# Kernel tuning notes

Hardware: AMD Instinct MI355X
Metric: run time of the kernel (lower is better)

## Reference

```python
import jax, jax.numpy as jnp
import numpy as np

N, E, F, D, G = 50000, 800000, 64, 64, 512
BN_EPS = 1e-5


def setup_inputs() -> dict:
    key = jax.random.key(0)
    ks = jax.random.split(key, 12)
    inp = {
        "x": jax.random.normal(ks[0], (N, F), dtype=jnp.float32),
        "edge_index": jax.random.randint(ks[1], (2, E), 0, N, dtype=jnp.int32),
        "batch": jnp.sort(jax.random.randint(ks[2], (N,), 0, G, dtype=jnp.int32)),
    }
    s = 0.05
    inp.update({
        "w1_a": jax.random.normal(ks[3], (F, D), jnp.float32) * s, "b1_a": jnp.zeros((D,), jnp.float32),
        "w1_b": jax.random.normal(ks[4], (D, D), jnp.float32) * s, "b1_b": jnp.zeros((D,), jnp.float32),
        "g1": jnp.ones((D,), jnp.float32), "be1": jnp.zeros((D,), jnp.float32),
        "w2_a": jax.random.normal(ks[5], (D, D), jnp.float32) * s, "b2_a": jnp.zeros((D,), jnp.float32),
        "w2_b": jax.random.normal(ks[6], (D, D), jnp.float32) * s, "b2_b": jnp.zeros((D,), jnp.float32),
        "g2": jnp.ones((D,), jnp.float32), "be2": jnp.zeros((D,), jnp.float32),
        "w3_a": jax.random.normal(ks[7], (D, D), jnp.float32) * s, "b3_a": jnp.zeros((D,), jnp.float32),
        "w3_b": jax.random.normal(ks[8], (D, D), jnp.float32) * s, "b3_b": jnp.zeros((D,), jnp.float32),
        "g3": jnp.ones((D,), jnp.float32), "be3": jnp.zeros((D,), jnp.float32),
        "w_lin0": jax.random.normal(ks[9], (D, 2 * D), jnp.float32) * s, "b_lin0": jnp.zeros((2 * D,), jnp.float32),
        "w_fc1": jax.random.normal(ks[10], (2 * D, D), jnp.float32) * s, "b_fc1": jnp.zeros((D,), jnp.float32),
    })
    return inp


def _gin_bn_layer(h, edge_index, w_a, b_a, w_b, b_b, gamma, beta):
    # GINConv (eps=0): nn(x + sum_{j->i} x_j); message = x[src] scattered to dst
    agg = jax.ops.segment_sum(h[edge_index[0]], edge_index[1], num_segments=h.shape[0])
    z = agg + h
    z = jnp.maximum(z @ w_a + b_a, 0.0) @ w_b + b_b  # inner MLP
    z = jnp.maximum(z, 0.0)                           # F.relu after conv
    mean = jnp.mean(z, axis=0)                        # BatchNorm1d, training stats
    var = jnp.mean((z - mean) ** 2, axis=0)
    return (z - mean) * jax.lax.rsqrt(var + BN_EPS) * gamma + beta


def reference(x, edge_index, batch,
              w1_a, b1_a, w1_b, b1_b, g1, be1,
              w2_a, b2_a, w2_b, b2_b, g2, be2,
              w3_a, b3_a, w3_b, b3_b, g3, be3,
              w_lin0, b_lin0, w_fc1, b_fc1):
    h = _gin_bn_layer(x, edge_index, w1_a, b1_a, w1_b, b1_b, g1, be1)
    h = _gin_bn_layer(h, edge_index, w2_a, b2_a, w2_b, b2_b, g2, be2)
    h = _gin_bn_layer(h, edge_index, w3_a, b3_a, w3_b, b3_b, g3, be3)
    xpool = jax.ops.segment_sum(h, batch, num_segments=G)  # global_add_pool [G, D]
    out = xpool @ w_lin0 + b_lin0                           # GINEncoder.lin0 -> [G, 2D]
    out = jnp.maximum(out @ w_fc1 + b_fc1, 0.0)             # relu(fc1); fc2 output is discarded (show_embedding=True)
    return out
```

## Files before the change

### kernel.cpp

```cpp
#include <hip/hip_runtime.h>

#define NN 50000
#define EE 800000
#define DD 64
#define GG 512
#define TILES 782
#define SCAN_BLOCKS 98

typedef __attribute__((ext_vector_type(8))) short short8;
typedef __attribute__((ext_vector_type(4))) float f32x4;

__device__ __forceinline__ float b2f(unsigned short u) {
    union { unsigned int i; float f; } c;
    c.i = ((unsigned int)u) << 16;
    return c.f;
}
__device__ __forceinline__ unsigned short f2b(float f) {
    union { float f; unsigned int i; } c;
    c.f = f;
    const unsigned int r = c.i + 0x7FFFu + ((c.i >> 16) & 1u);
    return (unsigned short)(r >> 16);
}
__device__ __forceinline__ int rfl(int v) { return __builtin_amdgcn_readfirstlane(v); }

__global__ __launch_bounds__(256) void prep_kernel(const float* __restrict__ x,
                                                   unsigned short* __restrict__ xbf,
                                                   int* __restrict__ counts,
                                                   float* __restrict__ zblock,
                                                   const float* __restrict__ w0,
                                                   const float* __restrict__ w1,
                                                   const float* __restrict__ w2,
                                                   const float* __restrict__ w3,
                                                   const float* __restrict__ w4,
                                                   const float* __restrict__ w5,
                                                   unsigned short* __restrict__ wfrag) {
    if (blockIdx.x >= 3209) {
        const float* ws[6] = {w0, w1, w2, w3, w4, w5};
        const int wi = blockIdx.x - 3209;
        const float* w = ws[wi];
        unsigned short* o = wfrag + wi * 4096;
        #pragma unroll
        for (int it = 0; it < 2; ++it) {
            const int idx = it * 256 + threadIdx.x;
            const int fid = idx >> 6, lane = idx & 63;
            const int kt = fid >> 2, nt = fid & 3;
            const int kbase = kt * 32 + (lane >> 4) * 8;
            const int n = nt * 16 + (lane & 15);
            #pragma unroll
            for (int j = 0; j < 8; ++j)
                o[idx * 8 + j] = f2b(w[(kbase + j) * 64 + n]);
        }
        return;
    }
    const int tid = blockIdx.x * 256 + threadIdx.x;
    if (tid < 800000) {
        const float4 v = ((const float4*)x)[tid];
        ushort4 o;
        o.x = f2b(v.x); o.y = f2b(v.y); o.z = f2b(v.z); o.w = f2b(v.w);
        ((ushort4*)xbf)[tid] = o;
    } else if (tid < 812500) {
        ((int4*)counts)[tid - 800000] = make_int4(0, 0, 0, 0);
    } else if (tid < 821460) {
        ((float4*)zblock)[tid - 812500] = make_float4(0.f, 0.f, 0.f, 0.f);
    }
}

__global__ __launch_bounds__(256) void hist_kernel(const int* __restrict__ ei,
                                                   int* __restrict__ counts) {
    const int e = blockIdx.x * blockDim.x + threadIdx.x;
    if (e < EE) atomicAdd(&counts[ei[EE + e]], 1);
}

__global__ __launch_bounds__(512) void scan1_kernel(const int* __restrict__ counts,
                                                    int* __restrict__ scanned,
                                                    int* __restrict__ bsum) {
    __shared__ int buf[512];
    const int i = blockIdx.x * 512 + threadIdx.x;
    const int v = (i < NN) ? counts[i] : 0;
    buf[threadIdx.x] = v;
    __syncthreads();
    for (int off = 1; off < 512; off <<= 1) {
        const int add = (threadIdx.x >= off) ? buf[threadIdx.x - off] : 0;
        __syncthreads();
        buf[threadIdx.x] += add;
        __syncthreads();
    }
    if (i < NN) scanned[i] = buf[threadIdx.x] - v;
    if (threadIdx.x == 511) bsum[blockIdx.x] = buf[511];
}

__global__ __launch_bounds__(512) void scan2_kernel(const int* __restrict__ scanned,
                                                    const int* __restrict__ bsum,
                                                    int* __restrict__ rowptr,
                                                    int* __restrict__ cursor) {
    __shared__ int red[128];
    if (threadIdx.x < 128)
        red[threadIdx.x] = (threadIdx.x < blockIdx.x) ? bsum[threadIdx.x] : 0;
    __syncthreads();
    for (int off = 64; off > 0; off >>= 1) {
        if (threadIdx.x < off) red[threadIdx.x] += red[threadIdx.x + off];
        __syncthreads();
    }
    const int offset = red[0];
    const int i = blockIdx.x * 512 + threadIdx.x;
    if (i < NN) {
        const int p = scanned[i] + offset;
        rowptr[i] = p;
        cursor[i] = p;
    }
    if (blockIdx.x == 0 && threadIdx.x == 0) rowptr[NN] = EE;
}

__global__ __launch_bounds__(256) void fill_kernel(const int* __restrict__ ei,
                                                   int* __restrict__ cursor,
                                                   int* __restrict__ col) {
    const int cls = blockIdx.x & 7;
    const int chunk = blockIdx.x >> 3;
    const int e0 = chunk * 3125;
    for (int e = e0 + threadIdx.x; e < e0 + 3125; e += 256) {
        const int dst = ei[EE + e];
        if (dst / 6250 == cls) {
            const int pos = atomicAdd(&cursor[dst], 1);
            col[pos] = ei[e];
        }
    }
}

__global__ __launch_bounds__(256, 4) void gather_kernel(const unsigned short* __restrict__ hin,
                                                        const int* __restrict__ rowptr,
                                                        const int* __restrict__ col,
                                                        const float* __restrict__ stats,
                                                        const float* __restrict__ ga,
                                                        const float* __restrict__ be,
                                                        const int apply,
                                                        unsigned short* __restrict__ z) {
    const int wv = (blockIdx.x * 256 + threadIdx.x) >> 6;
    const int lane = threadIdx.x & 63;
    const int row = rfl(wv);
    if (row >= NN) return;

    float scl = 1.0f, sft = 0.0f;
    if (apply) {
        float s = 0.f, sq = 0.f;
        #pragma unroll
        for (int k = 0; k < 8; ++k) {
            s += stats[k * 128 + lane];
            sq += stats[k * 128 + 64 + lane];
        }
        const float mean = s * (1.0f / NN);
        const float var = sq * (1.0f / NN) - mean * mean;
        scl = ga[lane] * rsqrtf(var + 1e-5f);
        sft = be[lane] - mean * scl;
    }

    const int beg = rfl(rowptr[row]);
    const int end = rfl(rowptr[row + 1]);
    const int deg = end - beg;
    float a[8];
    #pragma unroll
    for (int i = 0; i < 8; ++i) a[i] = 0.f;
    a[0] = b2f(hin[row * 64 + lane]);

    if (deg <= 16) {
        const int safeb = (beg < EE) ? beg : 0;
        int c[16];
        #pragma unroll
        for (int i = 0; i < 16; ++i) {
            const int jj = (i < deg) ? (beg + i) : safeb;
            c[i] = rfl(col[jj]);
        }
        float hv[16];
        #pragma unroll
        for (int i = 0; i < 16; ++i) hv[i] = b2f(hin[c[i] * 64 + lane]);
        #pragma unroll
        for (int i = 0; i < 16; ++i) a[i & 7] += (i < deg) ? hv[i] : 0.f;
    } else if (deg <= 24) {
        int c[24];
        #pragma unroll
        for (int i = 0; i < 24; ++i) {
            const int jj = (i < deg) ? (beg + i) : beg;
            c[i] = rfl(col[jj]);
        }
        float hv[24];
        #pragma unroll
        for (int i = 0; i < 24; ++i) hv[i] = b2f(hin[c[i] * 64 + lane]);
        #pragma unroll
        for (int i = 0; i < 24; ++i) a[i & 7] += (i < deg) ? hv[i] : 0.f;
    } else if (deg <= 32) {
        int c[32];
        #pragma unroll
        for (int i = 0; i < 32; ++i) {
            const int jj = (i < deg) ? (beg + i) : beg;
            c[i] = rfl(col[jj]);
        }
        float hv[32];
        #pragma unroll
        for (int i = 0; i < 32; ++i) hv[i] = b2f(hin[c[i] * 64 + lane]);
        #pragma unroll
        for (int i = 0; i < 32; ++i) a[i & 7] += (i < deg) ? hv[i] : 0.f;
    } else {
        int j = beg;
        for (; j + 16 <= end; j += 16) {
            int c[16];
            #pragma unroll
            for (int i = 0; i < 16; ++i) c[i] = rfl(col[j + i]);
            float hv[16];
            #pragma unroll
            for (int i = 0; i < 16; ++i) hv[i] = b2f(hin[c[i] * 64 + lane]);
            #pragma unroll
            for (int i = 0; i < 16; ++i) a[i & 7] += hv[i];
        }
        if (j < end) {
            int c[16];
            #pragma unroll
            for (int i = 0; i < 16; ++i) {
                const int jj = (j + i < end) ? (j + i) : beg;
                c[i] = rfl(col[jj]);
            }
            float hv[16];
            #pragma unroll
            for (int i = 0; i < 16; ++i) hv[i] = b2f(hin[c[i] * 64 + lane]);
            #pragma unroll
            for (int i = 0; i < 16; ++i) a[i & 7] += (j + i < end) ? hv[i] : 0.f;
        }
    }
    const float sum = ((a[0] + a[1]) + (a[2] + a[3])) + ((a[4] + a[5]) + (a[6] + a[7]));
    z[row * 64 + lane] = f2b(fmaf(sum, scl, (float)(deg + 1) * sft));
}

__global__ __launch_bounds__(256, 2) void mlp_kernel(const unsigned short* __restrict__ z,
                                                     const unsigned short* __restrict__ wfa,
                                                     const float* __restrict__ ba,
                                                     const unsigned short* __restrict__ wfb,
                                                     const float* __restrict__ bb,
                                                     unsigned short* __restrict__ tout,
                                                     float* __restrict__ stats) {
    __shared__ unsigned short ldsT[4][16][72];
    __shared__ float red[512];

    const int wave = threadIdx.x >> 6;
    const int lane = threadIdx.x & 63;
    const int quad = lane >> 4;
    const int l15 = lane & 15;
    const int rowbase = blockIdx.x * 64 + wave * 16;
    const bool valid = rowbase < NN;

    short8 wA[8], wB[8];
    #pragma unroll
    for (int f = 0; f < 8; ++f) {
        wA[f] = *(const short8*)(wfa + (f * 64 + lane) * 8);
        wB[f] = *(const short8*)(wfb + (f * 64 + lane) * 8);
    }
    float biasA[4], biasB[4];
    #pragma unroll
    for (int nt = 0; nt < 4; ++nt) {
        biasA[nt] = ba[nt * 16 + l15];
        biasB[nt] = bb[nt * 16 + l15];
    }

    const int arow = valid ? (rowbase + l15) : 0;
    const short8 a0 = *(const short8*)(z + arow * 64 + quad * 8);
    const short8 a1 = *(const short8*)(z + arow * 64 + 32 + quad * 8);

    f32x4 acc[4];
    #pragma unroll
    for (int nt = 0; nt < 4; ++nt) {
        f32x4 c = {0.f, 0.f, 0.f, 0.f};
        c = __builtin_amdgcn_mfma_f32_16x16x32_bf16(a0, wA[nt], c, 0, 0, 0);
        c = __builtin_amdgcn_mfma_f32_16x16x32_bf16(a1, wA[4 + nt], c, 0, 0, 0);
        acc[nt] = c;
    }
    #pragma unroll
    for (int nt = 0; nt < 4; ++nt)
        #pragma unroll
        for (int r = 0; r < 4; ++r)
            ldsT[wave][quad * 4 + r][nt * 16 + l15] =
                f2b(fmaxf(acc[nt][r] + biasA[nt], 0.f));

    const short8 y0 = *(const short8*)(&ldsT[wave][l15][quad * 8]);
    const short8 y1 = *(const short8*)(&ldsT[wave][l15][32 + quad * 8]);

    #pragma unroll
    for (int nt = 0; nt < 4; ++nt) {
        f32x4 c = {0.f, 0.f, 0.f, 0.f};
        c = __builtin_amdgcn_mfma_f32_16x16x32_bf16(y0, wB[nt], c, 0, 0, 0);
        c = __builtin_amdgcn_mfma_f32_16x16x32_bf16(y1, wB[4 + nt], c, 0, 0, 0);
        acc[nt] = c;
    }
    #pragma unroll
    for (int nt = 0; nt < 4; ++nt)
        #pragma unroll
        for (int r = 0; r < 4; ++r)
            ldsT[wave][quad * 4 + r][nt * 16 + l15] =
                f2b(fmaxf(acc[nt][r] + biasB[nt], 0.f));

    {
        float s = 0.f, sq = 0.f;
        if (valid) {
            #pragma unroll 4
            for (int r = 0; r < 16; ++r) {
                const float v = b2f(ldsT[wave][r][lane]);
                s += v;
                sq += v * v;
            }
        }
        red[wave * 128 + lane] = s;
        red[wave * 128 + 64 + lane] = sq;
    }
    __syncthreads();

    if (threadIdx.x < 128) {
        const float tot = red[threadIdx.x] + red[128 + threadIdx.x] +
                          red[256 + threadIdx.x] + red[384 + threadIdx.x];
        atomicAdd(&stats[(blockIdx.x & 7) * 128 + threadIdx.x], tot);
    }

    #pragma unroll
    for (int m = 0; m < 4; ++m) {
        const int g = m * 256 + threadIdx.x;
        const int r = g >> 4;
        const int f4 = (g & 15) * 4;
        const int grow = blockIdx.x * 64 + r;
        if (grow < NN)
            *(ushort4*)(tout + grow * 64 + f4) =
                *(const ushort4*)(&ldsT[r >> 4][r & 15][f4]);
    }
}

__global__ __launch_bounds__(256) void pool_kernel(const unsigned short* __restrict__ t,
                                                   const int* __restrict__ batch,
                                                   const float* __restrict__ stats,
                                                   const float* __restrict__ ga,
                                                   const float* __restrict__ be,
                                                   float* __restrict__ xpool) {
    const int wv = (blockIdx.x * 256 + threadIdx.x) >> 6;
    const int lane = threadIdx.x & 63;

    float s = 0.f, sq = 0.f;
    #pragma unroll
    for (int k = 0; k < 8; ++k) {
        s += stats[k * 128 + lane];
        sq += stats[k * 128 + 64 + lane];
    }
    const float mean = s * (1.0f / NN);
    const float var = sq * (1.0f / NN) - mean * mean;
    const float scl = ga[lane] * rsqrtf(var + 1e-5f);
    const float sft = be[lane] - mean * scl;

    const int r0 = wv * 64;
    if (r0 >= NN) return;
    const int r1 = min(r0 + 64, NN);
    int gprev = batch[r0];
    float acc = 0.f;
    for (int r = r0; r < r1; ++r) {
        const int g = batch[r];
        if (g != gprev) {
            __hip_atomic_fetch_add(&xpool[gprev * 64 + lane], acc,
                                   __ATOMIC_RELAXED, __HIP_MEMORY_SCOPE_AGENT);
            acc = 0.f;
            gprev = g;
        }
        acc += fmaf(b2f(t[r * 64 + lane]), scl, sft);
    }
    __hip_atomic_fetch_add(&xpool[gprev * 64 + lane], acc,
                           __ATOMIC_RELAXED, __HIP_MEMORY_SCOPE_AGENT);
}

__global__ __launch_bounds__(128) void head_kernel(const float* __restrict__ xpool,
                                                   const float* __restrict__ w0,
                                                   const float* __restrict__ b0,
                                                   const float* __restrict__ w1,
                                                   const float* __restrict__ b1,
                                                   float* __restrict__ out) {
    __shared__ float xp[64];
    __shared__ float midl[128];
    const int g = blockIdx.x;
    const int t = threadIdx.x;
    if (t < 64) xp[t] = xpool[g * 64 + t];
    __syncthreads();
    float acc = b0[t];
    #pragma unroll 8
    for (int k = 0; k < 64; ++k) acc = fmaf(xp[k], w0[k * 128 + t], acc);
    midl[t] = acc;
    __syncthreads();
    if (t < 64) {
        float a2 = b1[t];
        #pragma unroll 8
        for (int k = 0; k < 128; ++k) a2 = fmaf(midl[k], w1[k * 64 + t], a2);
        out[g * 64 + t] = fmaxf(a2, 0.f);
    }
}

extern "C" void kernel_launch(void* const* d_in, const int* in_sizes, int n_in,
                              void* d_out, int out_size, void* d_ws, size_t ws_size,
                              hipStream_t stream) {
    const float* x = (const float*)d_in[0];
    const int* ei = (const int*)d_in[1];
    const int* batch = (const int*)d_in[2];

    int* ibase   = (int*)d_ws;
    int* counts  = ibase;
    int* scanned = ibase + 50000;
    int* rowptr  = ibase + 100000;
    int* cursor  = ibase + 150004;
    int* bsum    = ibase + 200004;
    int* col     = ibase + 200132;
    float* fbase = (float*)d_ws + 1000192;
    float* stats = fbase;
    float* xpool = stats + 3072;
    unsigned short* zbf  = (unsigned short*)(fbase + 35856 + 128);
    unsigned short* xbf  = zbf + 3200000;
    unsigned short* t0bf = xbf + 3200000;
    unsigned short* t1bf = t0bf + 3200000;
    unsigned short* wfrag = t1bf + 3200000;

    prep_kernel<<<3215, 256, 0, stream>>>(x, xbf, counts, stats,
                                          (const float*)d_in[3], (const float*)d_in[5],
                                          (const float*)d_in[9], (const float*)d_in[11],
                                          (const float*)d_in[15], (const float*)d_in[17],
                                          wfrag);
    hist_kernel<<<(EE + 255) / 256, 256, 0, stream>>>(ei, counts);
    scan1_kernel<<<SCAN_BLOCKS, 512, 0, stream>>>(counts, scanned, bsum);
    scan2_kernel<<<SCAN_BLOCKS, 512, 0, stream>>>(scanned, bsum, rowptr, cursor);
    fill_kernel<<<2048, 256, 0, stream>>>(ei, cursor, col);

    const unsigned short* hcur = xbf;
    unsigned short* touts[3] = {t0bf, t1bf, t0bf};
    for (int l = 0; l < 3; ++l) {
        const float* ba = (const float*)d_in[3 + l * 6 + 1];
        const float* bb = (const float*)d_in[3 + l * 6 + 3];
        const float* gp = (const float*)d_in[3 + (l ? (l - 1) : 0) * 6 + 4];
        const float* bp = (const float*)d_in[3 + (l ? (l - 1) : 0) * 6 + 5];

        gather_kernel<<<12500, 256, 0, stream>>>(hcur, rowptr, col,
                                                 stats + (l ? (l - 1) : 0) * 1024,
                                                 gp, bp, l > 0, zbf);
        mlp_kernel<<<TILES, 256, 0, stream>>>(zbf,
                                              wfrag + (l * 2 + 0) * 4096, ba,
                                              wfrag + (l * 2 + 1) * 4096, bb,
                                              touts[l], stats + l * 1024);
        hcur = touts[l];
    }

    pool_kernel<<<(TILES + 3) / 4, 256, 0, stream>>>(
        t0bf, batch, stats + 2048,
        (const float*)d_in[19], (const float*)d_in[20], xpool);
    head_kernel<<<GG, 128, 0, stream>>>(
        xpool, (const float*)d_in[21], (const float*)d_in[22],
        (const float*)d_in[23], (const float*)d_in[24], (float*)d_out);
}
```

Measured before the change: 314.8 us.

## Split each wave into four sub-groups gathering neighbor rows with vectorized loads

The gather kernel now splits each 64-lane wave into four 16-lane groups. Each group loads a full 64-feature neighbor row with 8-byte ushort4 loads, and the four partial sums are reduced with cross-lane shuffles. Column indices are loaded once per wave and broadcast with shuffles instead of one readfirstlane per edge. Out-of-range slots point at a zeroed row, which the prep kernel now also clears, rather than being masked. Occupancy is raised to 8 blocks per CU. The goal is fewer, wider memory instructions and more rows in flight, at the cost of extra shuffles and reduction work.

```diff
diff --git a/kernel.cpp b/kernel.cpp
--- a/kernel.cpp
+++ b/kernel.cpp
@@ -22,6 +22,10 @@
     return (unsigned short)(r >> 16);
 }
 __device__ __forceinline__ int rfl(int v) { return __builtin_amdgcn_readfirstlane(v); }
+
+__device__ __forceinline__ void acc4(float* acc, ushort4 v) {
+    acc[0] += b2f(v.x); acc[1] += b2f(v.y); acc[2] += b2f(v.z); acc[3] += b2f(v.w);
+}
 
 __global__ __launch_bounds__(256) void prep_kernel(const float* __restrict__ x,
                                                    unsigned short* __restrict__ xbf,
@@ -60,7 +64,7 @@
         ((ushort4*)xbf)[tid] = o;
     } else if (tid < 812500) {
         ((int4*)counts)[tid - 800000] = make_int4(0, 0, 0, 0);
-    } else if (tid < 821460) {
+    } else if (tid < 821468) {
         ((float4*)zblock)[tid - 812500] = make_float4(0.f, 0.f, 0.f, 0.f);
     }
 }
@@ -126,20 +130,23 @@
     }
 }
 
-__global__ __launch_bounds__(256, 4) void gather_kernel(const unsigned short* __restrict__ hin,
+__global__ __launch_bounds__(256, 8) void gather_kernel(const unsigned short* __restrict__ hin,
                                                         const int* __restrict__ rowptr,
                                                         const int* __restrict__ col,
                                                         const float* __restrict__ stats,
                                                         const float* __restrict__ ga,
                                                         const float* __restrict__ be,
                                                         const int apply,
+                                                        const unsigned short* __restrict__ zrow,
                                                         unsigned short* __restrict__ z) {
     const int wv = (blockIdx.x * 256 + threadIdx.x) >> 6;
     const int lane = threadIdx.x & 63;
     const int row = rfl(wv);
     if (row >= NN) return;
-
-    float scl = 1.0f, sft = 0.0f;
+    const int sub = lane >> 4;
+    const int fg = lane & 15;
+
+    float scl[4], sft[4];
     if (apply) {
         float s = 0.f, sq = 0.f;
         #pragma unroll
@@ -149,83 +156,97 @@
         }
         const float mean = s * (1.0f / NN);
         const float var = sq * (1.0f / NN) - mean * mean;
-        scl = ga[lane] * rsqrtf(var + 1e-5f);
-        sft = be[lane] - mean * scl;
+        const float sc = ga[lane] * rsqrtf(var + 1e-5f);
+        const float sf = be[lane] - mean * sc;
+        #pragma unroll
+        for (int j = 0; j < 4; ++j) {
+            scl[j] = __shfl(sc, fg * 4 + j);
+            sft[j] = __shfl(sf, fg * 4 + j);
+        }
+    } else {
+        #pragma unroll
+        for (int j = 0; j < 4; ++j) { scl[j] = 1.0f; sft[j] = 0.0f; }
     }
 
     const int beg = rfl(rowptr[row]);
     const int end = rfl(rowptr[row + 1]);
     const int deg = end - beg;
-    float a[8];
-    #pragma unroll
-    for (int i = 0; i < 8; ++i) a[i] = 0.f;
-    a[0] = b2f(hin[row * 64 + lane]);
+
+    float acc[4];
+    {
+        const unsigned short* ps = (sub == 0) ? (hin + row * 64) : zrow;
+        const ushort4 sv = *(const ushort4*)(ps + fg * 4);
+        acc[0] = b2f(sv.x); acc[1] = b2f(sv.y); acc[2] = b2f(sv.z); acc[3] = b2f(sv.w);
+    }
 
     if (deg <= 16) {
-        const int safeb = (beg < EE) ? beg : 0;
-        int c[16];
-        #pragma unroll
-        for (int i = 0; i < 16; ++i) {
-            const int jj = (i < deg) ? (beg + i) : safeb;
-            c[i] = rfl(col[jj]);
-        }
-        float hv[16];
-        #pragma unroll
-        for (int i = 0; i < 16; ++i) hv[i] = b2f(hin[c[i] * 64 + lane]);
-        #pragma unroll
-        for (int i = 0; i < 16; ++i) a[i & 7] += (i < deg) ? hv[i] : 0.f;
-    } else if (deg <= 24) {
-        int c[24];
-        #pragma unroll
-        for (int i = 0; i < 24; ++i) {
-            const int jj = (i < deg) ? (beg + i) : beg;
-            c[i] = rfl(col[jj]);
-        }
-        float hv[24];
-        #pragma unroll
-        for (int i = 0; i < 24; ++i) hv[i] = b2f(hin[c[i] * 64 + lane]);
-        #pragma unroll
-        for (int i = 0; i < 24; ++i) a[i & 7] += (i < deg) ? hv[i] : 0.f;
+        const int cv = col[beg + (lane & 15)];
+        ushort4 hv[4];
+        #pragma unroll
+        for (int s = 0; s < 4; ++s) {
+            const int n = s * 4 + sub;
+            const int cr = __shfl(cv, n);
+            const unsigned short* pr = (n < deg) ? (hin + cr * 64) : zrow;
+            hv[s] = *(const ushort4*)(pr + fg * 4);
+        }
+        #pragma unroll
+        for (int s = 0; s < 4; ++s) acc4(acc, hv[s]);
     } else if (deg <= 32) {
-        int c[32];
-        #pragma unroll
-        for (int i = 0; i < 32; ++i) {
-            const int jj = (i < deg) ? (beg + i) : beg;
-            c[i] = rfl(col[jj]);
-        }
-        float hv[32];
-        #pragma unroll
-        for (int i = 0; i < 32; ++i) hv[i] = b2f(hin[c[i] * 64 + lane]);
-        #pragma unroll
-        for (int i = 0; i < 32; ++i) a[i & 7] += (i < deg) ? hv[i] : 0.f;
+        const int cv = col[beg + (lane & 31)];
+        ushort4 hv[8];
+        #pragma unroll
+        for (int s = 0; s < 8; ++s) {
+            const int n = s * 4 + sub;
+            const int cr = __shfl(cv, n);
+            const unsigned short* pr = (n < deg) ? (hin + cr * 64) : zrow;
+            hv[s] = *(const ushort4*)(pr + fg * 4);
+        }
+        #pragma unroll
+        for (int s = 0; s < 8; ++s) acc4(acc, hv[s]);
     } else {
-        int j = beg;
-        for (; j + 16 <= end; j += 16) {
-            int c[16];
+        int base = beg;
+        for (; base + 32 <= end; base += 32) {
+            const int cv = col[base + (lane & 31)];
+            ushort4 hv[8];
             #pragma unroll
-            for (int i = 0; i < 16; ++i) c[i] = rfl(col[j + i]);
-            float hv[16];
+            for (int s = 0; s < 8; ++s) {
+                const int cr = __shfl(cv, s * 4 + sub);
+                hv[s] = *(const ushort4*)(hin + cr * 64 + fg * 4);
+            }
             #pragma unroll
-            for (int i = 0; i < 16; ++i) hv[i] = b2f(hin[c[i] * 64 + lane]);
+            for (int s = 0; s < 8; ++s) acc4(acc, hv[s]);
+        }
+        if (base < end) {
+            const int rem = end - base;
+            const int cv = col[base + (lane & 31)];
+            ushort4 hv[8];
             #pragma unroll
-            for (int i = 0; i < 16; ++i) a[i & 7] += hv[i];
-        }
-        if (j < end) {
-            int c[16];
+            for (int s = 0; s < 8; ++s) {
+                const int n = s * 4 + sub;
+                const int cr = __shfl(cv, n);
+                const unsigned short* pr = (n < rem) ? (hin + cr * 64) : zrow;
+                hv[s] = *(const ushort4*)(pr + fg * 4);
+            }
             #pragma unroll
-            for (int i = 0; i < 16; ++i) {
-                const int jj = (j + i < end) ? (j + i) : beg;
-                c[i] = rfl(col[jj]);
-            }
-            float hv[16];
-            #pragma unroll
-            for (int i = 0; i < 16; ++i) hv[i] = b2f(hin[c[i] * 64 + lane]);
-            #pragma unroll
-            for (int i = 0; i < 16; ++i) a[i & 7] += (j + i < end) ? hv[i] : 0.f;
-        }
-    }
-    const float sum = ((a[0] + a[1]) + (a[2] + a[3])) + ((a[4] + a[5]) + (a[6] + a[7]));
-    z[row * 64 + lane] = f2b(fmaf(sum, scl, (float)(deg + 1) * sft));
+            for (int s = 0; s < 8; ++s) acc4(acc, hv[s]);
+        }
+    }
+
+    #pragma unroll
+    for (int j = 0; j < 4; ++j) {
+        acc[j] += __shfl_xor(acc[j], 16);
+        acc[j] += __shfl_xor(acc[j], 32);
+    }
+
+    if (sub == 0) {
+        const float dsft = (float)(deg + 1);
+        ushort4 o;
+        o.x = f2b(fmaf(acc[0], scl[0], dsft * sft[0]));
+        o.y = f2b(fmaf(acc[1], scl[1], dsft * sft[1]));
+        o.z = f2b(fmaf(acc[2], scl[2], dsft * sft[2]));
+        o.w = f2b(fmaf(acc[3], scl[3], dsft * sft[3]));
+        *(ushort4*)(z + row * 64 + fg * 4) = o;
+    }
 }
 
 __global__ __launch_bounds__(256, 2) void mlp_kernel(const unsigned short* __restrict__ z,
@@ -408,6 +429,7 @@
     float* fbase = (float*)d_ws + 1000192;
     float* stats = fbase;
     float* xpool = stats + 3072;
+    const unsigned short* zrow = (const unsigned short*)(fbase + 35840);
     unsigned short* zbf  = (unsigned short*)(fbase + 35856 + 128);
     unsigned short* xbf  = zbf + 3200000;
     unsigned short* t0bf = xbf + 3200000;
@@ -434,7 +456,7 @@
 
         gather_kernel<<<12500, 256, 0, stream>>>(hcur, rowptr, col,
                                                  stats + (l ? (l - 1) : 0) * 1024,
-                                                 gp, bp, l > 0, zbf);
+                                                 gp, bp, l > 0, zrow, zbf);
         mlp_kernel<<<TILES, 256, 0, stream>>>(zbf,
                                               wfrag + (l * 2 + 0) * 4096, ba,
                                               wfrag + (l * 2 + 1) * 4096, bb,
```

Measured after the change: 319.7 us. Within noise of the previous version (+1.6%).

## Fuse neighbor gather and MLP into one per-layer kernel with LDS weights

Applied to the files above, without the earlier changes.

Merges the gather kernel and the MLP kernel into a single layer kernel. Each wave gathers 16 rows sequentially into an LDS z-tile, and weight fragments are staged in LDS instead of registers. This removes the z round-trip through global memory and one launch per layer. In exchange, gather parallelism drops from one wave per row (12500 blocks) to 782 blocks with 16 serial rows per wave, which reduces latency hiding for the random gathers. The 17–32 degree specialisations are also removed.

```diff
diff --git a/kernel.cpp b/kernel.cpp
--- a/kernel.cpp
+++ b/kernel.cpp
@@ -126,18 +126,35 @@
     }
 }
 
-__global__ __launch_bounds__(256, 4) void gather_kernel(const unsigned short* __restrict__ hin,
-                                                        const int* __restrict__ rowptr,
-                                                        const int* __restrict__ col,
-                                                        const float* __restrict__ stats,
-                                                        const float* __restrict__ ga,
-                                                        const float* __restrict__ be,
-                                                        const int apply,
-                                                        unsigned short* __restrict__ z) {
-    const int wv = (blockIdx.x * 256 + threadIdx.x) >> 6;
+__global__ __launch_bounds__(256, 4) void layer_kernel(const unsigned short* __restrict__ hin,
+                                                       const int* __restrict__ rowptr,
+                                                       const int* __restrict__ col,
+                                                       const float* __restrict__ stats,
+                                                       const float* __restrict__ ga,
+                                                       const float* __restrict__ be,
+                                                       const int apply,
+                                                       const unsigned short* __restrict__ wfa,
+                                                       const float* __restrict__ ba,
+                                                       const unsigned short* __restrict__ wfb,
+                                                       const float* __restrict__ bb,
+                                                       unsigned short* __restrict__ tout,
+                                                       float* __restrict__ statsOut) {
+    __shared__ unsigned short wlds[8192];
+    __shared__ unsigned short ztile[64][72];
+    __shared__ unsigned short ldsT[4][16][72];
+    __shared__ float red[512];
+
+    const int wave = threadIdx.x >> 6;
     const int lane = threadIdx.x & 63;
-    const int row = rfl(wv);
-    if (row >= NN) return;
+    const int quad = lane >> 4;
+    const int l15 = lane & 15;
+
+    #pragma unroll
+    for (int i = 0; i < 2; ++i) {
+        const int idx = i * 256 + threadIdx.x;
+        ((short8*)wlds)[idx] = ((const short8*)wfa)[idx];
+        ((short8*)(wlds + 4096))[idx] = ((const short8*)wfb)[idx];
+    }
 
     float scl = 1.0f, sft = 0.0f;
     if (apply) {
@@ -153,104 +170,6 @@
         sft = be[lane] - mean * scl;
     }
 
-    const int beg = rfl(rowptr[row]);
-    const int end = rfl(rowptr[row + 1]);
-    const int deg = end - beg;
-    float a[8];
-    #pragma unroll
-    for (int i = 0; i < 8; ++i) a[i] = 0.f;
-    a[0] = b2f(hin[row * 64 + lane]);
-
-    if (deg <= 16) {
-        const int safeb = (beg < EE) ? beg : 0;
-        int c[16];
-        #pragma unroll
-        for (int i = 0; i < 16; ++i) {
-            const int jj = (i < deg) ? (beg + i) : safeb;
-            c[i] = rfl(col[jj]);
-        }
-        float hv[16];
-        #pragma unroll
-        for (int i = 0; i < 16; ++i) hv[i] = b2f(hin[c[i] * 64 + lane]);
-        #pragma unroll
-        for (int i = 0; i < 16; ++i) a[i & 7] += (i < deg) ? hv[i] : 0.f;
-    } else if (deg <= 24) {
-        int c[24];
-        #pragma unroll
-        for (int i = 0; i < 24; ++i) {
-            const int jj = (i < deg) ? (beg + i) : beg;
-            c[i] = rfl(col[jj]);
-        }
-        float hv[24];
-        #pragma unroll
-        for (int i = 0; i < 24; ++i) hv[i] = b2f(hin[c[i] * 64 + lane]);
-        #pragma unroll
-        for (int i = 0; i < 24; ++i) a[i & 7] += (i < deg) ? hv[i] : 0.f;
-    } else if (deg <= 32) {
-        int c[32];
-        #pragma unroll
-        for (int i = 0; i < 32; ++i) {
-            const int jj = (i < deg) ? (beg + i) : beg;
-            c[i] = rfl(col[jj]);
-        }
-        float hv[32];
-        #pragma unroll
-        for (int i = 0; i < 32; ++i) hv[i] = b2f(hin[c[i] * 64 + lane]);
-        #pragma unroll
-        for (int i = 0; i < 32; ++i) a[i & 7] += (i < deg) ? hv[i] : 0.f;
-    } else {
-        int j = beg;
-        for (; j + 16 <= end; j += 16) {
-            int c[16];
-            #pragma unroll
-            for (int i = 0; i < 16; ++i) c[i] = rfl(col[j + i]);
-            float hv[16];
-            #pragma unroll
-            for (int i = 0; i < 16; ++i) hv[i] = b2f(hin[c[i] * 64 + lane]);
-            #pragma unroll
-            for (int i = 0; i < 16; ++i) a[i & 7] += hv[i];
-        }
-        if (j < end) {
-            int c[16];
-            #pragma unroll
-            for (int i = 0; i < 16; ++i) {
-                const int jj = (j + i < end) ? (j + i) : beg;
-                c[i] = rfl(col[jj]);
-            }
-            float hv[16];
-            #pragma unroll
-            for (int i = 0; i < 16; ++i) hv[i] = b2f(hin[c[i] * 64 + lane]);
-            #pragma unroll
-            for (int i = 0; i < 16; ++i) a[i & 7] += (j + i < end) ? hv[i] : 0.f;
-        }
-    }
-    const float sum = ((a[0] + a[1]) + (a[2] + a[3])) + ((a[4] + a[5]) + (a[6] + a[7]));
-    z[row * 64 + lane] = f2b(fmaf(sum, scl, (float)(deg + 1) * sft));
-}
-
-__global__ __launch_bounds__(256, 2) void mlp_kernel(const unsigned short* __restrict__ z,
-                                                     const unsigned short* __restrict__ wfa,
-                                                     const float* __restrict__ ba,
-                                                     const unsigned short* __restrict__ wfb,
-                                                     const float* __restrict__ bb,
-                                                     unsigned short* __restrict__ tout,
-                                                     float* __restrict__ stats) {
-    __shared__ unsigned short ldsT[4][16][72];
-    __shared__ float red[512];
-
-    const int wave = threadIdx.x >> 6;
-    const int lane = threadIdx.x & 63;
-    const int quad = lane >> 4;
-    const int l15 = lane & 15;
-    const int rowbase = blockIdx.x * 64 + wave * 16;
-    const bool valid = rowbase < NN;
-
-    short8 wA[8], wB[8];
-    #pragma unroll
-    for (int f = 0; f < 8; ++f) {
-        wA[f] = *(const short8*)(wfa + (f * 64 + lane) * 8);
-        wB[f] = *(const short8*)(wfb + (f * 64 + lane) * 8);
-    }
     float biasA[4], biasB[4];
     #pragma unroll
     for (int nt = 0; nt < 4; ++nt) {
@@ -258,16 +177,78 @@
         biasB[nt] = bb[nt * 16 + l15];
     }
 
-    const int arow = valid ? (rowbase + l15) : 0;
-    const short8 a0 = *(const short8*)(z + arow * 64 + quad * 8);
-    const short8 a1 = *(const short8*)(z + arow * 64 + 32 + quad * 8);
+    const int base = blockIdx.x * 64 + wave * 16;
+    for (int i = 0; i < 16; ++i) {
+        const int row = base + i;
+        if (row < NN) {
+            const int beg = rfl(rowptr[row]);
+            const int end = rfl(rowptr[row + 1]);
+            const int deg = end - beg;
+            float a[8];
+            #pragma unroll
+            for (int q = 0; q < 8; ++q) a[q] = 0.f;
+            a[0] = b2f(hin[row * 64 + lane]);
+
+            if (deg <= 16) {
+                const int safeb = (beg < EE) ? beg : 0;
+                int c[16];
+                #pragma unroll
+                for (int t = 0; t < 16; ++t) {
+                    const int jj = (t < deg) ? (beg + t) : safeb;
+                    c[t] = rfl(col[jj]);
+                }
+                float hv[16];
+                #pragma unroll
+                for (int t = 0; t < 16; ++t) hv[t] = b2f(hin[c[t] * 64 + lane]);
+                #pragma unroll
+                for (int t = 0; t < 16; ++t) a[t & 7] += (t < deg) ? hv[t] : 0.f;
+            } else {
+                int j = beg;
+                for (; j + 16 <= end; j += 16) {
+                    int c[16];
+                    #pragma unroll
+                    for (int t = 0; t < 16; ++t) c[t] = rfl(col[j + t]);
+                    float hv[16];
+                    #pragma unroll
+                    for (int t = 0; t < 16; ++t) hv[t] = b2f(hin[c[t] * 64 + lane]);
+                    #pragma unroll
+                    for (int t = 0; t < 16; ++t) a[t & 7] += hv[t];
+                }
+                if (j < end) {
+                    int c[16];
+                    #pragma unroll
+                    for (int t = 0; t < 16; ++t) {
+                        const int jj = (j + t < end) ? (j + t) : beg;
+                        c[t] = rfl(col[jj]);
+                    }
+                    float hv[16];
+                    #pragma unroll
+                    for (int t = 0; t < 16; ++t) hv[t] = b2f(hin[c[t] * 64 + lane]);
+                    #pragma unroll
+                    for (int t = 0; t < 16; ++t) a[t & 7] += (j + t < end) ? hv[t] : 0.f;
+                }
+            }
+            const float sum = ((a[0] + a[1]) + (a[2] + a[3])) + ((a[4] + a[5]) + (a[6] + a[7]));
+            ztile[wave * 16 + i][lane] = f2b(fmaf(sum, scl, (float)(deg + 1) * sft));
+        } else {
+            ztile[wave * 16 + i][lane] = 0;
+        }
+    }
+    __syncthreads();
+
+    const bool valid = base < NN;
+    const int rloc = wave * 16 + l15;
+    const short8 a0 = *(const short8*)(&ztile[rloc][quad * 8]);
+    const short8 a1 = *(const short8*)(&ztile[rloc][32 + quad * 8]);
 
     f32x4 acc[4];
     #pragma unroll
     for (int nt = 0; nt < 4; ++nt) {
         f32x4 c = {0.f, 0.f, 0.f, 0.f};
-        c = __builtin_amdgcn_mfma_f32_16x16x32_bf16(a0, wA[nt], c, 0, 0, 0);
-        c = __builtin_amdgcn_mfma_f32_16x16x32_bf16(a1, wA[4 + nt], c, 0, 0, 0);
+        c = __builtin_amdgcn_mfma_f32_16x16x32_bf16(
+                a0, *(const short8*)(&wlds[(nt * 64 + lane) * 8]), c, 0, 0, 0);
+        c = __builtin_amdgcn_mfma_f32_16x16x32_bf16(
+                a1, *(const short8*)(&wlds[((4 + nt) * 64 + lane) * 8]), c, 0, 0, 0);
         acc[nt] = c;
     }
     #pragma unroll
@@ -283,8 +264,10 @@
     #pragma unroll
     for (int nt = 0; nt < 4; ++nt) {
         f32x4 c = {0.f, 0.f, 0.f, 0.f};
-        c = __builtin_amdgcn_mfma_f32_16x16x32_bf16(y0, wB[nt], c, 0, 0, 0);
-        c = __builtin_amdgcn_mfma_f32_16x16x32_bf16(y1, wB[4 + nt], c, 0, 0, 0);
+        c = __builtin_amdgcn_mfma_f32_16x16x32_bf16(
+                y0, *(const short8*)(&wlds[4096 + (nt * 64 + lane) * 8]), c, 0, 0, 0);
+        c = __builtin_amdgcn_mfma_f32_16x16x32_bf16(
+                y1, *(const short8*)(&wlds[4096 + ((4 + nt) * 64 + lane) * 8]), c, 0, 0, 0);
         acc[nt] = c;
     }
     #pragma unroll
@@ -312,7 +295,7 @@
     if (threadIdx.x < 128) {
         const float tot = red[threadIdx.x] + red[128 + threadIdx.x] +
                           red[256 + threadIdx.x] + red[384 + threadIdx.x];
-        atomicAdd(&stats[(blockIdx.x & 7) * 128 + threadIdx.x], tot);
+        atomicAdd(&statsOut[(blockIdx.x & 7) * 128 + threadIdx.x], tot);
     }
 
     #pragma unroll
@@ -432,13 +415,12 @@
         const float* gp = (const float*)d_in[3 + (l ? (l - 1) : 0) * 6 + 4];
         const float* bp = (const float*)d_in[3 + (l ? (l - 1) : 0) * 6 + 5];
 
-        gather_kernel<<<12500, 256, 0, stream>>>(hcur, rowptr, col,
-                                                 stats + (l ? (l - 1) : 0) * 1024,
-                                                 gp, bp, l > 0, zbf);
-        mlp_kernel<<<TILES, 256, 0, stream>>>(zbf,
-                                              wfrag + (l * 2 + 0) * 4096, ba,
-                                              wfrag + (l * 2 + 1) * 4096, bb,
-                                              touts[l], stats + l * 1024);
+        layer_kernel<<<TILES, 256, 0, stream>>>(hcur, rowptr, col,
+                                                stats + (l ? (l - 1) : 0) * 1024,
+                                                gp, bp, l > 0,
+                                                wfrag + (l * 2 + 0) * 4096, ba,
+                                                wfrag + (l * 2 + 1) * 4096, bb,
+                                                touts[l], stats + l * 1024);
         hcur = touts[l];
     }
 
```

Result: slower. 358.1 us (+13.7%).

## Fuse CSR build into one grid-synced kernel and fold pooling into last MLP

Applied to the files above, without the earlier changes.

Replaces the histogram, two-pass scan and fill kernels with one persistent 256-block kernel. It uses atomic grid barriers and a wave-level scan with an atomic base offset, so row starts come from per-row counts instead of a rowptr array. The final layer's MLP kernel now pools its rows straight into xpool and skips writing activations. The BatchNorm affine is applied in the head kernel, using per-graph counts found by binary search over batch. This removes several launches and a full pass over the last activation. The cost is a spin-barrier that can deadlock if not all blocks are co-resident, and row order in the CSR that is no longer deterministic.

```diff
diff --git a/kernel.cpp b/kernel.cpp
--- a/kernel.cpp
+++ b/kernel.cpp
@@ -2,10 +2,9 @@
 
 #define NN 50000
 #define EE 800000
-#define DD 64
 #define GG 512
 #define TILES 782
-#define SCAN_BLOCKS 98
+#define CSRB 256
 
 typedef __attribute__((ext_vector_type(8))) short short8;
 typedef __attribute__((ext_vector_type(4))) float f32x4;
@@ -23,9 +22,16 @@
 }
 __device__ __forceinline__ int rfl(int v) { return __builtin_amdgcn_readfirstlane(v); }
 
+__device__ __forceinline__ int lowb(const int* b, int v) {
+    int lo = 0, hi = NN;
+    while (lo < hi) { const int m = (lo + hi) >> 1; if (b[m] < v) lo = m + 1; else hi = m; }
+    return lo;
+}
+
 __global__ __launch_bounds__(256) void prep_kernel(const float* __restrict__ x,
                                                    unsigned short* __restrict__ xbf,
                                                    int* __restrict__ counts,
+                                                   int* __restrict__ ctrl,
                                                    float* __restrict__ zblock,
                                                    const float* __restrict__ w0,
                                                    const float* __restrict__ w1,
@@ -34,9 +40,9 @@
                                                    const float* __restrict__ w4,
                                                    const float* __restrict__ w5,
                                                    unsigned short* __restrict__ wfrag) {
-    if (blockIdx.x >= 3209) {
+    if (blockIdx.x >= 3210) {
         const float* ws[6] = {w0, w1, w2, w3, w4, w5};
-        const int wi = blockIdx.x - 3209;
+        const int wi = blockIdx.x - 3210;
         const float* w = ws[wi];
         unsigned short* o = wfrag + wi * 4096;
         #pragma unroll
@@ -60,74 +66,83 @@
         ((ushort4*)xbf)[tid] = o;
     } else if (tid < 812500) {
         ((int4*)counts)[tid - 800000] = make_int4(0, 0, 0, 0);
-    } else if (tid < 821460) {
-        ((float4*)zblock)[tid - 812500] = make_float4(0.f, 0.f, 0.f, 0.f);
-    }
-}
-
-__global__ __launch_bounds__(256) void hist_kernel(const int* __restrict__ ei,
-                                                   int* __restrict__ counts) {
-    const int e = blockIdx.x * blockDim.x + threadIdx.x;
-    if (e < EE) atomicAdd(&counts[ei[EE + e]], 1);
-}
-
-__global__ __launch_bounds__(512) void scan1_kernel(const int* __restrict__ counts,
-                                                    int* __restrict__ scanned,
-                                                    int* __restrict__ bsum) {
-    __shared__ int buf[512];
-    const int i = blockIdx.x * 512 + threadIdx.x;
-    const int v = (i < NN) ? counts[i] : 0;
-    buf[threadIdx.x] = v;
-    __syncthreads();
-    for (int off = 1; off < 512; off <<= 1) {
-        const int add = (threadIdx.x >= off) ? buf[threadIdx.x - off] : 0;
-        __syncthreads();
-        buf[threadIdx.x] += add;
-        __syncthreads();
-    }
-    if (i < NN) scanned[i] = buf[threadIdx.x] - v;
-    if (threadIdx.x == 511) bsum[blockIdx.x] = buf[511];
-}
-
-__global__ __launch_bounds__(512) void scan2_kernel(const int* __restrict__ scanned,
-                                                    const int* __restrict__ bsum,
-                                                    int* __restrict__ rowptr,
-                                                    int* __restrict__ cursor) {
-    __shared__ int red[128];
-    if (threadIdx.x < 128)
-        red[threadIdx.x] = (threadIdx.x < blockIdx.x) ? bsum[threadIdx.x] : 0;
-    __syncthreads();
-    for (int off = 64; off > 0; off >>= 1) {
-        if (threadIdx.x < off) red[threadIdx.x] += red[threadIdx.x + off];
-        __syncthreads();
-    }
-    const int offset = red[0];
-    const int i = blockIdx.x * 512 + threadIdx.x;
-    if (i < NN) {
-        const int p = scanned[i] + offset;
-        rowptr[i] = p;
-        cursor[i] = p;
-    }
-    if (blockIdx.x == 0 && threadIdx.x == 0) rowptr[NN] = EE;
-}
-
-__global__ __launch_bounds__(256) void fill_kernel(const int* __restrict__ ei,
-                                                   int* __restrict__ cursor,
-                                                   int* __restrict__ col) {
-    const int cls = blockIdx.x & 7;
-    const int chunk = blockIdx.x >> 3;
-    const int e0 = chunk * 3125;
-    for (int e = e0 + threadIdx.x; e < e0 + 3125; e += 256) {
-        const int dst = ei[EE + e];
-        if (dst / 6250 == cls) {
-            const int pos = atomicAdd(&cursor[dst], 1);
-            col[pos] = ei[e];
-        }
-    }
+    } else if (tid < 812756) {
+        ((int4*)ctrl)[tid - 812500] = make_int4(0, 0, 0, 0);
+    } else if (tid < 821716) {
+        ((float4*)zblock)[tid - 812756] = make_float4(0.f, 0.f, 0.f, 0.f);
+    }
+}
+
+__global__ __launch_bounds__(256, 4) void csr_kernel(const int* __restrict__ ei,
+                                                     int* __restrict__ counts,
+                                                     int* __restrict__ rowbeg,
+                                                     int* __restrict__ cursor,
+                                                     int* __restrict__ ctrl,
+                                                     int* __restrict__ col) {
+    const int gtid = blockIdx.x * 256 + threadIdx.x;
+    const int lane = threadIdx.x & 63;
+
+#define CBAR(slot) do {                                                        \
+        __syncthreads();                                                       \
+        if (threadIdx.x == 0) {                                                \
+            __hip_atomic_fetch_add(&ctrl[slot], 1, __ATOMIC_RELAXED,           \
+                                   __HIP_MEMORY_SCOPE_AGENT);                  \
+            int sp = 0;                                                        \
+            while (__hip_atomic_load(&ctrl[slot], __ATOMIC_RELAXED,            \
+                                     __HIP_MEMORY_SCOPE_AGENT) < CSRB) {       \
+                __builtin_amdgcn_s_sleep(2);                                   \
+                if (++sp > (1 << 20)) break;                                   \
+            }                                                                  \
+        }                                                                      \
+        __syncthreads();                                                       \
+    } while (0)
+
+    for (int e = gtid; e < EE; e += CSRB * 256) atomicAdd(&counts[ei[EE + e]], 1);
+    CBAR(128);
+
+    {
+        const int gw = gtid >> 6;
+        if (gw < TILES) {
+            const int r = gw * 64 + lane;
+            const int cnt = (r < NN) ? counts[r] : 0;
+            int incl = cnt;
+            #pragma unroll
+            for (int off = 1; off < 64; off <<= 1) {
+                const int tv = __shfl_up(incl, off);
+                if (lane >= off) incl += tv;
+            }
+            const int tot = __shfl(incl, 63);
+            int base = 0;
+            if (lane == 63)
+                base = __hip_atomic_fetch_add(&ctrl[64], tot, __ATOMIC_RELAXED,
+                                              __HIP_MEMORY_SCOPE_AGENT);
+            base = __shfl(base, 63);
+            if (r < NN) {
+                const int b0 = base + incl - cnt;
+                rowbeg[r] = b0;
+                __hip_atomic_store(&cursor[r], b0, __ATOMIC_RELAXED,
+                                   __HIP_MEMORY_SCOPE_AGENT);
+            }
+        }
+    }
+    CBAR(160);
+
+    {
+        const int cls = blockIdx.x & 7;
+        for (int e = (blockIdx.x >> 3) * 256 + threadIdx.x; e < EE; e += 32 * 256) {
+            const int dst = ei[EE + e];
+            if (dst / 6250 == cls) {
+                const int pos = atomicAdd(&cursor[dst], 1);
+                col[pos] = ei[e];
+            }
+        }
+    }
+#undef CBAR
 }
 
 __global__ __launch_bounds__(256, 4) void gather_kernel(const unsigned short* __restrict__ hin,
-                                                        const int* __restrict__ rowptr,
+                                                        const int* __restrict__ rowbeg,
+                                                        const int* __restrict__ counts,
                                                         const int* __restrict__ col,
                                                         const float* __restrict__ stats,
                                                         const float* __restrict__ ga,
@@ -153,9 +168,9 @@
         sft = be[lane] - mean * scl;
     }
 
-    const int beg = rfl(rowptr[row]);
-    const int end = rfl(rowptr[row + 1]);
-    const int deg = end - beg;
+    const int beg = rfl(rowbeg[row]);
+    const int deg = rfl(counts[row]);
+    const int end = beg + deg;
     float a[8];
     #pragma unroll
     for (int i = 0; i < 8; ++i) a[i] = 0.f;
@@ -234,7 +249,10 @@
                                                      const unsigned short* __restrict__ wfb,
                                                      const float* __restrict__ bb,
                                                      unsigned short* __restrict__ tout,
-                                                     float* __restrict__ stats) {
+                                                     float* __restrict__ stats,
+                                                     const int* __restrict__ batch,
+                                                     float* __restrict__ xpool,
+                                                     const int dopool) {
     __shared__ unsigned short ldsT[4][16][72];
     __shared__ float red[512];
 
@@ -315,58 +333,41 @@
         atomicAdd(&stats[(blockIdx.x & 7) * 128 + threadIdx.x], tot);
     }
 
-    #pragma unroll
-    for (int m = 0; m < 4; ++m) {
-        const int g = m * 256 + threadIdx.x;
-        const int r = g >> 4;
-        const int f4 = (g & 15) * 4;
-        const int grow = blockIdx.x * 64 + r;
-        if (grow < NN)
-            *(ushort4*)(tout + grow * 64 + f4) =
-                *(const ushort4*)(&ldsT[r >> 4][r & 15][f4]);
-    }
-}
-
-__global__ __launch_bounds__(256) void pool_kernel(const unsigned short* __restrict__ t,
+    if (!dopool) {
+        #pragma unroll
+        for (int m = 0; m < 4; ++m) {
+            const int g = m * 256 + threadIdx.x;
+            const int r = g >> 4;
+            const int f4 = (g & 15) * 4;
+            const int grow = blockIdx.x * 64 + r;
+            if (grow < NN)
+                *(ushort4*)(tout + grow * 64 + f4) =
+                    *(const ushort4*)(&ldsT[r >> 4][r & 15][f4]);
+        }
+    } else if (valid) {
+        int gprev = rfl(batch[rowbase]);
+        float acc2 = 0.f;
+        for (int i = 0; i < 16; ++i) {
+            const int row = rowbase + i;
+            if (row >= NN) break;
+            const int g = rfl(batch[row]);
+            const float v = b2f(ldsT[wave][i][lane]);
+            if (g != gprev) {
+                atomicAdd(&xpool[gprev * 64 + lane], acc2);
+                acc2 = 0.f;
+                gprev = g;
+            }
+            acc2 += v;
+        }
+        atomicAdd(&xpool[gprev * 64 + lane], acc2);
+    }
+}
+
+__global__ __launch_bounds__(128) void head_kernel(const float* __restrict__ xpool,
                                                    const int* __restrict__ batch,
                                                    const float* __restrict__ stats,
-                                                   const float* __restrict__ ga,
-                                                   const float* __restrict__ be,
-                                                   float* __restrict__ xpool) {
-    const int wv = (blockIdx.x * 256 + threadIdx.x) >> 6;
-    const int lane = threadIdx.x & 63;
-
-    float s = 0.f, sq = 0.f;
-    #pragma unroll
-    for (int k = 0; k < 8; ++k) {
-        s += stats[k * 128 + lane];
-        sq += stats[k * 128 + 64 + lane];
-    }
-    const float mean = s * (1.0f / NN);
-    const float var = sq * (1.0f / NN) - mean * mean;
-    const float scl = ga[lane] * rsqrtf(var + 1e-5f);
-    const float sft = be[lane] - mean * scl;
-
-    const int r0 = wv * 64;
-    if (r0 >= NN) return;
-    const int r1 = min(r0 + 64, NN);
-    int gprev = batch[r0];
-    float acc = 0.f;
-    for (int r = r0; r < r1; ++r) {
-        const int g = batch[r];
-        if (g != gprev) {
-            __hip_atomic_fetch_add(&xpool[gprev * 64 + lane], acc,
-                                   __ATOMIC_RELAXED, __HIP_MEMORY_SCOPE_AGENT);
-            acc = 0.f;
-            gprev = g;
-        }
-        acc += fmaf(b2f(t[r * 64 + lane]), scl, sft);
-    }
-    __hip_atomic_fetch_add(&xpool[gprev * 64 + lane], acc,
-                           __ATOMIC_RELAXED, __HIP_MEMORY_SCOPE_AGENT);
-}
-
-__global__ __launch_bounds__(128) void head_kernel(const float* __restrict__ xpool,
+                                                   const float* __restrict__ g3,
+                                                   const float* __restrict__ be3,
                                                    const float* __restrict__ w0,
                                                    const float* __restrict__ b0,
                                                    const float* __restrict__ w1,
@@ -376,7 +377,20 @@
     __shared__ float midl[128];
     const int g = blockIdx.x;
     const int t = threadIdx.x;
-    if (t < 64) xp[t] = xpool[g * 64 + t];
+    if (t < 64) {
+        float s = 0.f, sq = 0.f;
+        #pragma unroll
+        for (int k = 0; k < 8; ++k) {
+            s += stats[k * 128 + t];
+            sq += stats[k * 128 + 64 + t];
+        }
+        const float mean = s * (1.0f / NN);
+        const float var = sq * (1.0f / NN) - mean * mean;
+        const float scl = g3[t] * rsqrtf(var + 1e-5f);
+        const float sft = be3[t] - mean * scl;
+        const int cnt = lowb(batch, g + 1) - lowb(batch, g);
+        xp[t] = fmaf(xpool[g * 64 + t], scl, (float)cnt * sft);
+    }
     __syncthreads();
     float acc = b0[t];
     #pragma unroll 8
@@ -400,29 +414,25 @@
 
     int* ibase   = (int*)d_ws;
     int* counts  = ibase;
-    int* scanned = ibase + 50000;
-    int* rowptr  = ibase + 100000;
-    int* cursor  = ibase + 150004;
-    int* bsum    = ibase + 200004;
-    int* col     = ibase + 200132;
-    float* fbase = (float*)d_ws + 1000192;
+    int* rowbeg  = ibase + 50000;
+    int* cursor  = ibase + 100000;
+    int* ctrl    = ibase + 150000;
+    int* col     = ibase + 151040;
+    float* fbase = (float*)d_ws + 951040;
     float* stats = fbase;
     float* xpool = stats + 3072;
-    unsigned short* zbf  = (unsigned short*)(fbase + 35856 + 128);
-    unsigned short* xbf  = zbf + 3200000;
-    unsigned short* t0bf = xbf + 3200000;
-    unsigned short* t1bf = t0bf + 3200000;
+    unsigned short* zbf   = (unsigned short*)(fbase + 35840);
+    unsigned short* xbf   = zbf + 3200000;
+    unsigned short* t0bf  = xbf + 3200000;
+    unsigned short* t1bf  = t0bf + 3200000;
     unsigned short* wfrag = t1bf + 3200000;
 
-    prep_kernel<<<3215, 256, 0, stream>>>(x, xbf, counts, stats,
+    prep_kernel<<<3216, 256, 0, stream>>>(x, xbf, counts, ctrl, stats,
                                           (const float*)d_in[3], (const float*)d_in[5],
                                           (const float*)d_in[9], (const float*)d_in[11],
                                           (const float*)d_in[15], (const float*)d_in[17],
                                           wfrag);
-    hist_kernel<<<(EE + 255) / 256, 256, 0, stream>>>(ei, counts);
-    scan1_kernel<<<SCAN_BLOCKS, 512, 0, stream>>>(counts, scanned, bsum);
-    scan2_kernel<<<SCAN_BLOCKS, 512, 0, stream>>>(scanned, bsum, rowptr, cursor);
-    fill_kernel<<<2048, 256, 0, stream>>>(ei, cursor, col);
+    csr_kernel<<<CSRB, 256, 0, stream>>>(ei, counts, rowbeg, cursor, ctrl, col);
 
     const unsigned short* hcur = xbf;
     unsigned short* touts[3] = {t0bf, t1bf, t0bf};
@@ -432,20 +442,20 @@
         const float* gp = (const float*)d_in[3 + (l ? (l - 1) : 0) * 6 + 4];
         const float* bp = (const float*)d_in[3 + (l ? (l - 1) : 0) * 6 + 5];
 
-        gather_kernel<<<12500, 256, 0, stream>>>(hcur, rowptr, col,
+        gather_kernel<<<12500, 256, 0, stream>>>(hcur, rowbeg, counts, col,
                                                  stats + (l ? (l - 1) : 0) * 1024,
                                                  gp, bp, l > 0, zbf);
         mlp_kernel<<<TILES, 256, 0, stream>>>(zbf,
                                               wfrag + (l * 2 + 0) * 4096, ba,
                                               wfrag + (l * 2 + 1) * 4096, bb,
-                                              touts[l], stats + l * 1024);
+                                              touts[l], stats + l * 1024,
+                                              batch, xpool, (l == 2) ? 1 : 0);
         hcur = touts[l];
     }
 
-    pool_kernel<<<(TILES + 3) / 4, 256, 0, stream>>>(
-        t0bf, batch, stats + 2048,
-        (const float*)d_in[19], (const float*)d_in[20], xpool);
     head_kernel<<<GG, 128, 0, stream>>>(
-        xpool, (const float*)d_in[21], (const float*)d_in[22],
+        xpool, batch, stats + 2048,
+        (const float*)d_in[19], (const float*)d_in[20],
+        (const float*)d_in[21], (const float*)d_in[22],
         (const float*)d_in[23], (const float*)d_in[24], (float*)d_out);
 }
```

Result: slower. 361.6 us (+14.9%).
